# Kernel optimization log

Hardware: AMD Instinct MI355X
Metric: run time of the kernel (lower is better)

## Reference

```python
import jax, jax.numpy as jnp
import numpy as np

PATCH = 4
WINDOW = 4
MAX_ROUNDS = 4
MIN_ROUNDS = 2
LAMBDA_P = 0.2
TOPK = 8


def _ln(x, g, b, eps=1e-5):
    m = x.mean(-1, keepdims=True)
    v = ((x - m) ** 2).mean(-1, keepdims=True)
    return (x - m) / jnp.sqrt(v + eps) * g + b


def _mlp(x, w1, b1, w2, b2):
    # Linear -> exact GELU -> Linear (matches nn.GELU default)
    return jax.nn.gelu(x @ w1 + b1, approximate=False) @ w2 + b2


def setup_inputs() -> dict:
    key = jax.random.key(0)
    ks = jax.random.split(key, 24)
    B, T, D, V = 16, 4096, 256, 256
    s = 0.02
    w = lambda i, shape: jax.random.normal(ks[i], shape, jnp.float32) * s
    z = lambda *shape: jnp.zeros(shape, jnp.float32)
    o = lambda *shape: jnp.ones(shape, jnp.float32)
    return {
        'x': jax.random.randint(ks[0], (B, T), 0, V),
        'emb': w(1, (V, D)), 'pos': w(2, (PATCH, D)),
        'gru_wih': w(3, (D, 3 * D)), 'gru_whh': w(4, (D, 3 * D)),
        'gru_bih': z(3 * D), 'gru_bhh': z(3 * D),
        'ln_p_g': o(D), 'ln_p_b': z(D),
        'sum_w': w(5, (D, D)), 'sum_b': z(D),
        'msg_w1': w(6, (2 * D, D)), 'msg_b1': z(D), 'msg_w2': w(7, (D, D)), 'msg_b2': z(D),
        'upd_w1': w(8, (2 * D, D)), 'upd_b1': z(D), 'upd_w2': w(9, (D, D)), 'upd_b2': z(D),
        'halt_w': w(10, (D, 1)), 'halt_b': z(1),
        'ln_mp_g': o(D), 'ln_mp_b': z(D),
        'q_w': w(11, (D, D)), 'q_b': z(D),
        'k_w': w(12, (D, D)), 'k_b': z(D),
        'v_w': w(13, (D, D)), 'v_b': z(D),
        'o_w': w(14, (D, D)), 'o_b': z(D),
        'bc_w': w(15, (D, D)), 'bc_b': z(D),
        'ln_f_g': o(D), 'ln_f_b': z(D),
        'head_w': w(16, (D, V)),
    }


def reference(x, emb, pos, gru_wih, gru_whh, gru_bih, gru_bhh, ln_p_g, ln_p_b,
              sum_w, sum_b, msg_w1, msg_b1, msg_w2, msg_b2, upd_w1, upd_b1,
              upd_w2, upd_b2, halt_w, halt_b, ln_mp_g, ln_mp_b, q_w, q_b,
              k_w, k_b, v_w, v_b, o_w, o_b, bc_w, bc_b, ln_f_g, ln_f_b, head_w):
    B, T = x.shape
    D = emb.shape[1]
    Np = T // PATCH  # T is divisible by PATCH for these shapes (no pad needed)

    # --- GRU patch processor over B*Np sequences of length PATCH ---
    tok = x.reshape(B * Np, PATCH)
    hseq = emb[tok] + pos[None]  # [BN, P, D]

    def gru_step(h, xt):
        gi = xt @ gru_wih + gru_bih
        gh = h @ gru_whh + gru_bhh
        ir, iz, inn = jnp.split(gi, 3, -1)
        hr, hz, hn = jnp.split(gh, 3, -1)
        r = jax.nn.sigmoid(ir + hr)
        zz = jax.nn.sigmoid(iz + hz)
        n = jnp.tanh(inn + r * hn)
        h = (1 - zz) * n + zz * h
        return h, h

    h0 = jnp.zeros((B * Np, D), hseq.dtype)
    _, gout = jax.lax.scan(gru_step, h0, jnp.swapaxes(hseq, 0, 1))
    local = _ln(jnp.swapaxes(gout, 0, 1), ln_p_g, ln_p_b).reshape(B, Np, PATCH, D)
    summaries = local.mean(2) @ sum_w + sum_b  # [B, Np, D]

    # --- Local message passing with ACT-style halting (fixed MAX_ROUNDS) ---
    h = summaries
    remaining = jnp.ones((B, Np, 1), h.dtype)
    out_mp = jnp.zeros_like(h)
    kl = jnp.zeros((), h.dtype)
    for step in range(MAX_ROUNDS):
        padded = jnp.pad(h, ((0, 0), (WINDOW, 0), (0, 0)))
        # neighbors: self plus previous WINDOW patches -> [B, Np, W+1, D]
        neigh = jnp.stack([padded[:, WINDOW - w:WINDOW - w + Np] for w in range(WINDOW + 1)], axis=2)
        self_exp = jnp.broadcast_to(h[:, :, None, :], neigh.shape)
        msgs = _mlp(jnp.concatenate([self_exp, neigh], -1), msg_w1, msg_b1, msg_w2, msg_b2).mean(2)
        h = _ln(h + _mlp(jnp.concatenate([h, msgs], -1), upd_w1, upd_b1, upd_w2, upd_b2), ln_mp_g, ln_mp_b)
        if step < MIN_ROUNDS:
            hp = jnp.zeros((B, Np, 1), h.dtype)
        else:
            hp = jax.nn.sigmoid(h.mean(1, keepdims=True) @ halt_w + halt_b)  # [B,1,1]
            hp = jnp.broadcast_to(hp, (B, Np, 1))
        if step == MAX_ROUNDS - 1:
            hp = jnp.ones_like(hp)
        out_mp = out_mp + remaining * hp * h
        remaining = remaining * (1 - hp)
        p_geom = LAMBDA_P * (1 - LAMBDA_P) ** step
        # F.kl_div(log(mean+eps), log(p_geom), log_target=True) = p*(log p - log(mean+eps))
        kl = kl + p_geom * (np.log(p_geom) - jnp.log(hp.mean() + 1e-8))
    kl = kl / MAX_ROUNDS

    # --- Sparse top-k causal retrieval ---
    q = out_mp @ q_w + q_b
    kk = out_mp @ k_w + k_b
    v = out_mp @ v_w + v_b
    scores = jnp.einsum('bnd,bmd->bnm', q, kk) / np.sqrt(D).astype(np.float32)
    causal = jnp.tril(jnp.ones((Np, Np), bool))
    neg = jnp.asarray(-jnp.inf, scores.dtype)
    scores = jnp.where(causal[None], scores, neg)
    vals, idx = jax.lax.top_k(scores, TOPK)  # [B, Np, k]
    bi = jnp.arange(B)[:, None, None]
    ni = jnp.arange(Np)[None, :, None]
    sparse = jnp.full_like(scores, neg).at[bi, ni, idx].set(vals)
    attn = jax.nn.softmax(sparse, axis=-1)
    retrieved = jnp.einsum('bnm,bmd->bnd', attn, v) @ o_w + o_b

    # --- Broadcast back to tokens and project ---
    combined = out_mp + retrieved
    broad = combined @ bc_w + bc_b
    final = (local + broad[:, :, None, :]).reshape(B, Np * PATCH, D)[:, :T]
    logits = _ln(final, ln_f_g, ln_f_b) @ head_w
    return logits, kl
```

## Files before the change

### kernel.cpp

```cpp
#include <hip/hip_runtime.h>
#include <math.h>


typedef __bf16 bf16_t;
typedef bf16_t bf16x8 __attribute__((ext_vector_type(8)));
typedef bf16_t bf16x4 __attribute__((ext_vector_type(4)));
typedef float f32x4 __attribute__((ext_vector_type(4)));

#define GF_BIAS 1
#define GF_GELU 4
#define GF_RES 8
#define GF_F32OUT 32

__device__ __forceinline__ float gelu_exact(float x) {
  return 0.5f * x * (1.0f + erff(x * 0.7071067811865475f));
}

__device__ __forceinline__ float sigm(float x) { return 1.f / (1.f + expf(-x)); }

__device__ __forceinline__ float wave_sum(float v) {
#pragma unroll
  for (int o = 32; o; o >>= 1) v += __shfl_xor(v, o, 64);
  return v;
}

__device__ __forceinline__ void gload16(const void* g, void* l) {
  __builtin_amdgcn_global_load_lds(
      (const __attribute__((address_space(1))) void*)g,
      (__attribute__((address_space(3))) void*)l, 16, 0, 0);
}

__device__ __forceinline__ unsigned long long skey(float s, int m) {
  unsigned u = __float_as_uint(s);
  u ^= (u & 0x80000000u) ? 0xFFFFFFFFu : 0x80000000u;
  return ((unsigned long long)u << 32) | (unsigned)(0x7FFFFFFF - m);
}

template<int FLAGS>
__global__ __launch_bounds__(256)
void gemm_bt(const bf16_t* __restrict__ A, const bf16_t* __restrict__ Bt,
             void* __restrict__ Cv, const float* __restrict__ bias,
             const bf16_t* __restrict__ res,
             int lda, int ldb, int ldc, int ldr)
{
  __shared__ __align__(16) bf16_t As[128][64];
  __shared__ __align__(16) bf16_t Bs[128][64];
  const int m0 = blockIdx.x * 128, n0 = blockIdx.y * 128;
  const int tid = threadIdx.x, lane = tid & 63, wave = tid >> 6;
  const int wm = (wave >> 1) << 6, wn = (wave & 1) << 6;
  const int lr = lane & 15, lg = lane >> 4;
  const int cx = lane & 7;

  const int srow = wave * 32 + (lane >> 3);
  const int scol = (((lane & 7) ^ ((lane >> 3) & 7)) * 8);
  const bf16_t* ga = A  + (long long)(m0 + srow) * lda + scol;
  const bf16_t* gb = Bt + (long long)(n0 + srow) * ldb + scol;
  char* lA = (char*)(&As[srow][0]) + (lane & 7) * 16;
  char* lB = (char*)(&Bs[srow][0]) + (lane & 7) * 16;

  f32x4 acc[4][4] = {};

#pragma unroll
  for (int kt = 0; kt < 4; kt++) {
    const int ko = kt * 64;
#pragma unroll
    for (int q = 0; q < 4; q++) {
      gload16(ga + (long long)q * 8 * lda + ko, lA + q * 1024);
      gload16(gb + (long long)q * 8 * ldb + ko, lB + q * 1024);
    }
    __syncthreads();
#pragma unroll
    for (int kk = 0; kk < 2; kk++) {
      const int co = ((kk * 4 + lg) ^ cx) << 4;
      bf16x8 af[4], bfv[4];
#pragma unroll
      for (int i = 0; i < 4; i++)
        af[i]  = *(const bf16x8*)((char*)As + (wm + i * 16 + lr) * 128 + co);
#pragma unroll
      for (int j = 0; j < 4; j++)
        bfv[j] = *(const bf16x8*)((char*)Bs + (wn + j * 16 + lr) * 128 + co);
#pragma unroll
      for (int i = 0; i < 4; i++)
#pragma unroll
        for (int j = 0; j < 4; j++)
          acc[i][j] = __builtin_amdgcn_mfma_f32_16x16x32_bf16(af[i], bfv[j], acc[i][j], 0, 0, 0);
    }
    if (kt < 3) __syncthreads();
  }

#pragma unroll
  for (int i = 0; i < 4; i++) {
#pragma unroll
    for (int j = 0; j < 4; j++) {
      const int col = n0 + wn + j * 16 + lr;
      const float bval = (FLAGS & GF_BIAS) ? bias[col] : 0.f;
#pragma unroll
      for (int e = 0; e < 4; e++) {
        const int row = m0 + wm + i * 16 + lg * 4 + e;
        float v = acc[i][j][e] + bval;
        if (FLAGS & GF_RES) v += (float)res[(long long)row * ldr + col];
        if (FLAGS & GF_GELU) v = gelu_exact(v);
        const long long ci = (long long)row * ldc + col;
        if (FLAGS & GF_F32OUT) ((float*)Cv)[ci] = v;
        else                   ((bf16_t*)Cv)[ci] = (bf16_t)v;
      }
    }
  }
}

template<int FLAGS>
__global__ __launch_bounds__(256)
void gemm64(const bf16_t* __restrict__ A, const bf16_t* __restrict__ Bt,
            void* __restrict__ Cv, const float* __restrict__ bias,
            const bf16_t* __restrict__ res,
            int lda, int ldb, int ldc, int ldr)
{
  __shared__ __align__(16) bf16_t As[64][64];
  __shared__ __align__(16) bf16_t Bs[64][64];
  const int m0 = blockIdx.x * 64, n0 = blockIdx.y * 64;
  const int tid = threadIdx.x, lane = tid & 63, wave = tid >> 6;
  const int wm = (wave >> 1) * 32, wn = (wave & 1) * 32;
  const int lr = lane & 15, lg = lane >> 4;
  const int cx = lane & 7;

  const int srow = tid >> 3;
  const int scol = (((tid & 7) ^ (srow & 7)) * 8);
  const bf16_t* ga = A  + (long long)(m0 + srow) * lda + scol;
  const bf16_t* gb = Bt + (long long)(n0 + srow) * ldb + scol;
  char* lA = (char*)As + tid * 16;
  char* lB = (char*)Bs + tid * 16;

  f32x4 acc[2][2] = {};

#pragma unroll
  for (int kt = 0; kt < 4; kt++) {
    const int ko = kt * 64;
    gload16(ga + ko, lA);
    gload16(ga + 32LL * lda + ko, lA + 4096);
    gload16(gb + ko, lB);
    gload16(gb + 32LL * ldb + ko, lB + 4096);
    __syncthreads();
#pragma unroll
    for (int kk = 0; kk < 2; kk++) {
      const int co = ((kk * 4 + lg) ^ cx) << 4;
      bf16x8 af[2], bfv[2];
#pragma unroll
      for (int i = 0; i < 2; i++)
        af[i]  = *(const bf16x8*)((char*)As + (wm + i * 16 + lr) * 128 + co);
#pragma unroll
      for (int j = 0; j < 2; j++)
        bfv[j] = *(const bf16x8*)((char*)Bs + (wn + j * 16 + lr) * 128 + co);
#pragma unroll
      for (int i = 0; i < 2; i++)
#pragma unroll
        for (int j = 0; j < 2; j++)
          acc[i][j] = __builtin_amdgcn_mfma_f32_16x16x32_bf16(af[i], bfv[j], acc[i][j], 0, 0, 0);
    }
    if (kt < 3) __syncthreads();
  }

#pragma unroll
  for (int i = 0; i < 2; i++) {
#pragma unroll
    for (int j = 0; j < 2; j++) {
      const int col = n0 + wn + j * 16 + lr;
      const float bval = (FLAGS & GF_BIAS) ? bias[col] : 0.f;
#pragma unroll
      for (int e = 0; e < 4; e++) {
        const int row = m0 + wm + i * 16 + lg * 4 + e;
        float v = acc[i][j][e] + bval;
        if (FLAGS & GF_RES) v += (float)res[(long long)row * ldr + col];
        if (FLAGS & GF_GELU) v = gelu_exact(v);
        const long long ci = (long long)row * ldc + col;
        if (FLAGS & GF_F32OUT) ((float*)Cv)[ci] = v;
        else                   ((bf16_t*)Cv)[ci] = (bf16_t)v;
      }
    }
  }
}

__global__ __launch_bounds__(256)
void k_fatopk(const bf16_t* __restrict__ QKV, bf16_t* __restrict__ O) {
  __shared__ unsigned long long cand[4][16][8];
  __shared__ float wrow[16][8];
  __shared__ int   irow[16][8];
  const int b = blockIdx.y;
  const int qw = (int)((blockIdx.x + ((unsigned)(b * 21) & 63u)) & 63u);
  const int tid = threadIdx.x;
  const int wid = tid >> 6;
  const int lane = tid & 63;
  const int lr = lane & 15, lg = lane >> 4;
  const bf16_t* Qp = QKV + (long long)b * (1024LL * 768);
  const bf16_t* Kp = Qp + 256;
  const bf16_t* Vp = Qp + 512;
  const int q0 = qw * 16;
  const int qrow = q0 + lr;

  bf16x8 bq[8];
#pragma unroll
  for (int s = 0; s < 8; s++)
    bq[s] = *(const bf16x8*)(Qp + (long long)qrow * 768 + s * 32 + lg * 8);

  unsigned long long kv[8] = {0ull, 0ull, 0ull, 0ull, 0ull, 0ull, 0ull, 0ull};

#define INS8(KEY) {                                                     \
    const unsigned long long k_ = (KEY);                                \
    if (k_ > kv[7]) {                                                   \
      kv[7] = k_;                                                       \
      _Pragma("unroll")                                                 \
      for (int j_ = 7; j_ > 0; j_--)                                    \
        if (kv[j_] > kv[j_-1]) {                                        \
          const unsigned long long t_ = kv[j_];                         \
          kv[j_] = kv[j_-1]; kv[j_-1] = t_;                             \
        }                                                               \
    }                                                                   \
  }

  const int klim = qw + 1;
  for (int kt = wid; kt < klim; kt += 4) {
    const bf16_t* ka = Kp + (long long)(kt * 16 + lr) * 768 + lg * 8;
    bf16x8 af[8];
#pragma unroll
    for (int s = 0; s < 8; s++) af[s] = *(const bf16x8*)(ka + s * 32);
    f32x4 a0 = {}, a1 = {};
#pragma unroll
    for (int s = 0; s < 8; s += 2) {
      a0 = __builtin_amdgcn_mfma_f32_16x16x32_bf16(af[s],     bq[s],     a0, 0, 0, 0);
      a1 = __builtin_amdgcn_mfma_f32_16x16x32_bf16(af[s + 1], bq[s + 1], a1, 0, 0, 0);
    }
#pragma unroll
    for (int e = 0; e < 4; e++) {
      const int m = kt * 16 + lg * 4 + e;
      if (m <= qrow) INS8(skey((a0[e] + a1[e]) * 0.0625f, m));
    }
  }
#undef INS8

#pragma unroll
  for (int r = 0; r < 8; r++) {
    unsigned long long mk = kv[0];
    unsigned long long ok = __shfl_xor(mk, 16, 64); if (ok > mk) mk = ok;
    ok = __shfl_xor(mk, 32, 64); if (ok > mk) mk = ok;
    if (lg == 0) cand[wid][lr][r] = mk;
    if (kv[0] == mk && mk != 0ull) {
#pragma unroll
      for (int j = 0; j < 7; j++) kv[j] = kv[j + 1];
      kv[7] = 0ull;
    }
  }
  __syncthreads();

  if (wid == 0) {
    unsigned long long kv2[8];
#pragma unroll
    for (int j = 0; j < 8; j++) kv2[j] = cand[lg][lr][j];
    float wv[8]; int wi[8];
#pragma unroll
    for (int r = 0; r < 8; r++) {
      unsigned long long mk = kv2[0];
      unsigned long long ok = __shfl_xor(mk, 16, 64); if (ok > mk) mk = ok;
      ok = __shfl_xor(mk, 32, 64); if (ok > mk) mk = ok;
      if (mk != 0ull) {
        unsigned hi = (unsigned)(mk >> 32);
        hi ^= (hi & 0x80000000u) ? 0x80000000u : 0xFFFFFFFFu;
        wv[r] = __uint_as_float(hi);
        wi[r] = 0x7FFFFFFF - (int)(unsigned)(mk & 0xFFFFFFFFu);
      } else {
        wv[r] = 0.f; wi[r] = -1;
      }
      if (kv2[0] == mk && mk != 0ull) {
#pragma unroll
        for (int j = 0; j < 7; j++) kv2[j] = kv2[j + 1];
        kv2[7] = 0ull;
      }
    }
    const float mx = wv[0];
    float w8[8]; float den = 0.f;
#pragma unroll
    for (int j = 0; j < 8; j++) {
      w8[j] = (wi[j] >= 0) ? expf(wv[j] - mx) : 0.f;
      den += w8[j];
    }
    const float inv = 1.f / den;
    if (lg == 0) {
#pragma unroll
      for (int j = 0; j < 8; j++) {
        wrow[lr][j] = w8[j] * inv;
        irow[lr][j] = wi[j];
      }
    }
  }
  __syncthreads();

  const int rr = wid * 4 + lg;
  const int c0 = (lane & 15) * 16;
  f32x4 av[4] = {};
#pragma unroll
  for (int j = 0; j < 8; j++) {
    const int idx = irow[rr][j];
    if (idx >= 0) {
      const float wj = wrow[rr][j];
      const bf16_t* vr = Vp + (long long)idx * 768 + c0;
      const bf16x8 v0 = *(const bf16x8*)vr;
      const bf16x8 v1 = *(const bf16x8*)(vr + 8);
#pragma unroll
      for (int e = 0; e < 4; e++) {
        av[0][e] = fmaf(wj, (float)v0[e],     av[0][e]);
        av[1][e] = fmaf(wj, (float)v0[4 + e], av[1][e]);
        av[2][e] = fmaf(wj, (float)v1[e],     av[2][e]);
        av[3][e] = fmaf(wj, (float)v1[4 + e], av[3][e]);
      }
    }
  }
  bf16_t* op = O + ((long long)b * 1024 + q0 + rr) * 256 + c0;
  bf16x8 o0, o1;
#pragma unroll
  for (int e = 0; e < 4; e++) {
    o0[e] = (bf16_t)av[0][e]; o0[4 + e] = (bf16_t)av[1][e];
    o1[e] = (bf16_t)av[2][e]; o1[4 + e] = (bf16_t)av[3][e];
  }
  *(bf16x8*)op = o0;
  *(bf16x8*)(op + 8) = o1;
}

struct TD { const float* src; bf16_t* dst; int N; int k0; int ld; };
struct PrepArgs {
  TD d[16];
  const float* emb; const float* pos; bf16_t* XE;
  const float* msg_b1; const float* msg_b2; const float* upd_w1; const float* upd_b1;
  const float* q_b; const float* k_b; const float* v_b;
  float* BIAS3; float* QKVB;
};

__global__ __launch_bounds__(256) void k_prep(PrepArgs pa) {
  const int y = blockIdx.y, x = blockIdx.x, d = threadIdx.x;
  if (y < 16) {
    TD t = pa.d[y];
    if (x >= t.N) return;
    if (t.k0 < 0) t.dst[(long long)x * 256 + d] = (bf16_t)t.src[(long long)x * t.ld + d];
    else          t.dst[(long long)x * 256 + d] = (bf16_t)t.src[(long long)(t.k0 + d) * t.ld + x];
  } else if (y == 16) {
    const int p = x >> 8, v = x & 255;
    pa.XE[(long long)x * 256 + d] = (bf16_t)(pa.emb[v * 256 + d] + pa.pos[p * 256 + d]);
  } else {
    if      (x == 0) pa.BIAS3[d] = pa.msg_b1[d];
    else if (x == 1) pa.BIAS3[256 + d] = 0.f;
    else if (x == 2) {
      float acc = pa.upd_b1[d];
      for (int k = 0; k < 256; k++) acc += pa.msg_b2[k] * pa.upd_w1[(long long)(256 + k) * 256 + d];
      pa.BIAS3[512 + d] = acc;
    }
    else if (x == 3) pa.QKVB[d] = pa.q_b[d];
    else if (x == 4) pa.QKVB[256 + d] = pa.k_b[d];
    else if (x == 5) pa.QKVB[512 + d] = pa.v_b[d];
  }
}

__global__ __launch_bounds__(64)
void k_gru_gate(const int* __restrict__ x, const bf16_t* __restrict__ gitab,
                const bf16_t* __restrict__ GH, const float* __restrict__ bhh,
                bf16_t* __restrict__ H, bf16_t* __restrict__ LOC, int t)
{
  const int s = blockIdx.x, lane = threadIdx.x, d0 = lane * 4;
  const int v = x[s * 4 + t];
  const bf16_t* gi = gitab + (long long)(t * 256 + v) * 768;
  const bf16x4 g_r = *(const bf16x4*)(gi + d0);
  const bf16x4 g_z = *(const bf16x4*)(gi + 256 + d0);
  const bf16x4 g_n = *(const bf16x4*)(gi + 512 + d0);
  float hr[4], hz[4], hn[4], hp[4];
  if (t == 0) {
#pragma unroll
    for (int e = 0; e < 4; e++) {
      hr[e] = bhh[d0 + e]; hz[e] = bhh[256 + d0 + e]; hn[e] = bhh[512 + d0 + e];
      hp[e] = 0.f;
    }
  } else {
    const bf16_t* gh = GH + (long long)s * 768;
    const bf16x4 a = *(const bf16x4*)(gh + d0);
    const bf16x4 b4 = *(const bf16x4*)(gh + 256 + d0);
    const bf16x4 c4 = *(const bf16x4*)(gh + 512 + d0);
    const bf16x4 hv = *(const bf16x4*)(H + (long long)s * 256 + d0);
#pragma unroll
    for (int e = 0; e < 4; e++) { hr[e] = a[e]; hz[e] = b4[e]; hn[e] = c4[e]; hp[e] = hv[e]; }
  }
  bf16x4 ho;
#pragma unroll
  for (int e = 0; e < 4; e++) {
    const float r = sigm((float)g_r[e] + hr[e]);
    const float zz = sigm((float)g_z[e] + hz[e]);
    const float nn = tanhf((float)g_n[e] + r * hn[e]);
    ho[e] = (bf16_t)((1.f - zz) * nn + zz * hp[e]);
  }
  *(bf16x4*)(H + (long long)s * 256 + d0) = ho;
  *(bf16x4*)(LOC + ((long long)s * 4 + t) * 256 + d0) = ho;
}

__global__ __launch_bounds__(64)
void k_ln(const bf16_t* __restrict__ X, const bf16_t* __restrict__ ADD, int addmode,
          bf16_t* __restrict__ OUT, const float* __restrict__ g,
          const float* __restrict__ b)
{
  const long long r = blockIdx.x;
  const int d0 = threadIdx.x * 4;
  const bf16x4 xv = *(const bf16x4*)(X + r * 256 + d0);
  float xf[4];
#pragma unroll
  for (int e = 0; e < 4; e++) xf[e] = (float)xv[e];
  if (addmode == 1) {
    const bf16x4 av = *(const bf16x4*)(ADD + r * 256 + d0);
#pragma unroll
    for (int e = 0; e < 4; e++) xf[e] += (float)av[e];
  } else if (addmode == 2) {
    const bf16x4 av = *(const bf16x4*)(ADD + (r >> 2) * 256 + d0);
#pragma unroll
    for (int e = 0; e < 4; e++) xf[e] += (float)av[e];
  }
  const float mean = wave_sum(xf[0] + xf[1] + xf[2] + xf[3]) * (1.f / 256.f);
  float q = 0.f;
#pragma unroll
  for (int e = 0; e < 4; e++) { const float dx = xf[e] - mean; q += dx * dx; }
  const float rstd = rsqrtf(wave_sum(q) * (1.f / 256.f) + 1e-5f);
  const float4 gv = *(const float4*)(g + d0);
  const float4 bv = *(const float4*)(b + d0);
  const float gg[4] = {gv.x, gv.y, gv.z, gv.w};
  const float bb[4] = {bv.x, bv.y, bv.z, bv.w};
  bf16x4 ov;
#pragma unroll
  for (int e = 0; e < 4; e++) ov[e] = (bf16_t)((xf[e] - mean) * rstd * gg[e] + bb[e]);
  *(bf16x4*)(OUT + r * 256 + d0) = ov;
}

__global__ __launch_bounds__(64)
void k_ln_out(const bf16_t* __restrict__ X, const bf16_t* __restrict__ ADD,
              bf16_t* __restrict__ OUTMP, const float* __restrict__ HP,
              const float* __restrict__ g, const float* __restrict__ b)
{
  const long long r = blockIdx.x;
  const int d0 = threadIdx.x * 4;
  const bf16x4 xv = *(const bf16x4*)(X + r * 256 + d0);
  const bf16x4 avv = *(const bf16x4*)(ADD + r * 256 + d0);
  float xf[4];
#pragma unroll
  for (int e = 0; e < 4; e++) xf[e] = (float)xv[e] + (float)avv[e];
  const float mean = wave_sum(xf[0] + xf[1] + xf[2] + xf[3]) * (1.f / 256.f);
  float q = 0.f;
#pragma unroll
  for (int e = 0; e < 4; e++) { const float dx = xf[e] - mean; q += dx * dx; }
  const float rstd = rsqrtf(wave_sum(q) * (1.f / 256.f) + 1e-5f);
  const float4 gv = *(const float4*)(g + d0);
  const float4 bv = *(const float4*)(b + d0);
  const float gg[4] = {gv.x, gv.y, gv.z, gv.w};
  const float bb[4] = {bv.x, bv.y, bv.z, bv.w};
  const float rem = 1.f - HP[(int)(r >> 10)];
  const bf16x4 pv = *(const bf16x4*)(OUTMP + r * 256 + d0);
  bf16x4 ov;
#pragma unroll
  for (int e = 0; e < 4; e++) {
    const float y = (xf[e] - mean) * rstd * gg[e] + bb[e];
    ov[e] = (bf16_t)((float)pv[e] + rem * y);
  }
  *(bf16x4*)(OUTMP + r * 256 + d0) = ov;
}

__global__ __launch_bounds__(64)
void k_lnp4(bf16_t* __restrict__ LOC, bf16_t* __restrict__ SUMB,
            const float* __restrict__ g, const float* __restrict__ b)
{
  const long long s = blockIdx.x;
  const int d0 = threadIdx.x * 4;
  const float4 gv = *(const float4*)(g + d0);
  const float4 bv = *(const float4*)(b + d0);
  const float gg[4] = {gv.x, gv.y, gv.z, gv.w};
  const float bb[4] = {bv.x, bv.y, bv.z, bv.w};
  float accd[4] = {0.f, 0.f, 0.f, 0.f};
#pragma unroll
  for (int t = 0; t < 4; t++) {
    bf16_t* row = LOC + (s * 4 + t) * 256 + d0;
    const bf16x4 xv = *(const bf16x4*)row;
    float xf[4];
#pragma unroll
    for (int e = 0; e < 4; e++) xf[e] = (float)xv[e];
    const float mean = wave_sum(xf[0] + xf[1] + xf[2] + xf[3]) * (1.f / 256.f);
    float q = 0.f;
#pragma unroll
    for (int e = 0; e < 4; e++) { const float dx = xf[e] - mean; q += dx * dx; }
    const float rstd = rsqrtf(wave_sum(q) * (1.f / 256.f) + 1e-5f);
    bf16x4 ov;
#pragma unroll
    for (int e = 0; e < 4; e++) {
      const float y = (xf[e] - mean) * rstd * gg[e] + bb[e];
      ov[e] = (bf16_t)y;
      accd[e] += y;
    }
    *(bf16x4*)row = ov;
  }
  bf16x4 sv;
#pragma unroll
  for (int e = 0; e < 4; e++) sv[e] = (bf16_t)(accd[e] * 0.25f);
  *(bf16x4*)(SUMB + s * 256 + d0) = sv;
}

__global__ __launch_bounds__(64)
void k_gelumix(const bf16_t* __restrict__ A3, bf16_t* __restrict__ G)
{
  const long long s = blockIdx.x;
  const int n = (int)(s & 1023);
  const int d0 = threadIdx.x * 4;
  const bf16x4 av = *(const bf16x4*)(A3 + s * 768 + d0);
  float a[4];
#pragma unroll
  for (int e = 0; e < 4; e++) a[e] = (float)av[e];
  float acc[4] = {0.f, 0.f, 0.f, 0.f};
  const bf16_t* bbase = A3 + s * 768 + 256 + d0;
#pragma unroll
  for (int w = 0; w <= 4; w++) {
    if (n >= w) {
      const bf16x4 bn = *(const bf16x4*)(bbase - (long long)w * 768);
#pragma unroll
      for (int e = 0; e < 4; e++) acc[e] += gelu_exact(a[e] + (float)bn[e]);
    } else {
#pragma unroll
      for (int e = 0; e < 4; e++) acc[e] += gelu_exact(a[e]);
    }
  }
  bf16x4 ov;
#pragma unroll
  for (int e = 0; e < 4; e++) ov[e] = (bf16_t)(acc[e] * 0.2f);
  *(bf16x4*)(G + s * 256 + d0) = ov;
}

__global__ __launch_bounds__(64)
void k_halt1(const bf16_t* __restrict__ Hm, float* __restrict__ PS) {
  const int c = blockIdx.x, b = blockIdx.y, d0 = threadIdx.x * 4;
  float acc[4] = {0.f, 0.f, 0.f, 0.f};
  const bf16_t* base = Hm + ((long long)b * 1024 + c * 32) * 256 + d0;
#pragma unroll 4
  for (int n = 0; n < 32; n++) {
    const bf16x4 hv = *(const bf16x4*)(base + (long long)n * 256);
#pragma unroll
    for (int e = 0; e < 4; e++) acc[e] += (float)hv[e];
  }
  float4 o4; o4.x = acc[0]; o4.y = acc[1]; o4.z = acc[2]; o4.w = acc[3];
  *(float4*)(PS + ((long long)b * 32 + c) * 256 + d0) = o4;
}

__global__ __launch_bounds__(64)
void k_halt2(const float* __restrict__ PS, const float* __restrict__ hw,
             const float* __restrict__ hb, float* __restrict__ HP) {
  const int b = blockIdx.x, d0 = threadIdx.x * 4;
  float acc[4] = {0.f, 0.f, 0.f, 0.f};
  for (int c = 0; c < 32; c++) {
    const float4 p4 = *(const float4*)(PS + ((long long)b * 32 + c) * 256 + d0);
    acc[0] += p4.x; acc[1] += p4.y; acc[2] += p4.z; acc[3] += p4.w;
  }
  const float4 w4 = *(const float4*)(hw + d0);
  float val = (acc[0] * w4.x + acc[1] * w4.y + acc[2] * w4.z + acc[3] * w4.w) * (1.f / 1024.f);
  val = wave_sum(val);
  if (threadIdx.x == 0) HP[b] = sigm(val + hb[0]);
}

__global__ void k_kl(const float* __restrict__ HP, float* __restrict__ out) {
  float s = 0.f;
  for (int b = 0; b < 16; b++) s += HP[b];
  const float hpm = s * (1.f / 16.f);
  const float l8 = logf(1e-8f);
  const float p0 = 0.2f, p1 = 0.16f, p2 = 0.128f, p3 = 0.1024f;
  const float kl = p0 * (logf(p0) - l8)
                 + p1 * (logf(p1) - l8)
                 + p2 * (logf(p2) - logf(hpm + 1e-8f))
                 + p3 * (logf(p3) - logf(1.f + 1e-8f));
  out[0] = kl * 0.25f;
}

__global__ __launch_bounds__(64)
void k_outmp(const bf16_t* __restrict__ Hm, const float* __restrict__ HP,
             bf16_t* __restrict__ O, int acc) {
  const long long s = blockIdx.x;
  const int d0 = threadIdx.x * 4;
  const int b = (int)(s >> 10);
  const float hp = HP[b];
  const bf16x4 hv = *(const bf16x4*)(Hm + s * 256 + d0);
  bf16x4 ov;
  if (acc) {
    const bf16x4 pv = *(const bf16x4*)(O + s * 256 + d0);
#pragma unroll
    for (int e = 0; e < 4; e++) ov[e] = (bf16_t)((float)pv[e] + (1.f - hp) * (float)hv[e]);
  } else {
#pragma unroll
    for (int e = 0; e < 4; e++) ov[e] = (bf16_t)(hp * (float)hv[e]);
  }
  *(bf16x4*)(O + s * 256 + d0) = ov;
}

extern "C" void kernel_launch(void* const* d_in, const int* in_sizes, int n_in,
                              void* d_out, int out_size, void* d_ws, size_t ws_size,
                              hipStream_t stream) {
  (void)in_sizes; (void)n_in; (void)ws_size;
  const int*   x      = (const int*)d_in[0];
  const float* emb    = (const float*)d_in[1];
  const float* pos    = (const float*)d_in[2];
  const float* wih    = (const float*)d_in[3];
  const float* whh    = (const float*)d_in[4];
  const float* bih    = (const float*)d_in[5];
  const float* bhh    = (const float*)d_in[6];
  const float* lnp_g  = (const float*)d_in[7];
  const float* lnp_b  = (const float*)d_in[8];
  const float* sum_w  = (const float*)d_in[9];
  const float* sum_b  = (const float*)d_in[10];
  const float* msg_w1 = (const float*)d_in[11];
  const float* msg_b1 = (const float*)d_in[12];
  const float* msg_w2 = (const float*)d_in[13];
  const float* msg_b2 = (const float*)d_in[14];
  const float* upd_w1 = (const float*)d_in[15];
  const float* upd_b1 = (const float*)d_in[16];
  const float* upd_w2 = (const float*)d_in[17];
  const float* upd_b2 = (const float*)d_in[18];
  const float* halt_w = (const float*)d_in[19];
  const float* halt_b = (const float*)d_in[20];
  const float* lnm_g  = (const float*)d_in[21];
  const float* lnm_b  = (const float*)d_in[22];
  const float* q_b    = (const float*)d_in[24];
  const float* k_b    = (const float*)d_in[26];
  const float* v_b    = (const float*)d_in[28];
  const float* o_b    = (const float*)d_in[30];
  const float* bc_b   = (const float*)d_in[32];
  const float* lnf_g  = (const float*)d_in[33];
  const float* lnf_b  = (const float*)d_in[34];

  char* base = (char*)d_ws;
  size_t off = 0;
  auto alloc = [&](size_t bytes) -> void* {
    void* p = (void*)(base + off);
    off += (bytes + 255) & ~(size_t)255;
    return p;
  };
  const size_t SL2 = 16384ull * 256 * 2;
  bf16_t* WIHT  = (bf16_t*)alloc(768 * 256 * 2);
  bf16_t* WHHT  = (bf16_t*)alloc(768 * 256 * 2);
  bf16_t* SUMT  = (bf16_t*)alloc(256 * 256 * 2);
  bf16_t* MW    = (bf16_t*)alloc(768 * 256 * 2);
  bf16_t* W2T   = (bf16_t*)alloc(256 * 256 * 2);
  bf16_t* W2NT  = (bf16_t*)alloc(256 * 256 * 2);
  bf16_t* UW1MT = (bf16_t*)alloc(256 * 256 * 2);
  bf16_t* UW2T  = (bf16_t*)alloc(256 * 256 * 2);
  bf16_t* WCB   = (bf16_t*)alloc(256 * 256 * 2);
  bf16_t* QKVW  = (bf16_t*)alloc(768 * 256 * 2);
  bf16_t* OT    = (bf16_t*)alloc(256 * 256 * 2);
  bf16_t* BCT   = (bf16_t*)alloc(256 * 256 * 2);
  bf16_t* HEADT = (bf16_t*)alloc(256 * 256 * 2);
  float*  BIAS3 = (float*)alloc(768 * 4);
  float*  QKVB  = (float*)alloc(768 * 4);
  bf16_t* XE    = (bf16_t*)alloc(1024ull * 256 * 2);
  bf16_t* GITAB = (bf16_t*)alloc(1024ull * 768 * 2);
  bf16_t* LOCb  = (bf16_t*)alloc(65536ull * 256 * 2);

  char*   SCR   = (char*)alloc(16ull * 1024 * 1024 * 4);
  bf16_t* GH    = (bf16_t*)SCR;
  bf16_t* H     = (bf16_t*)(SCR + 25165824);
  bf16_t* SUMB  = (bf16_t*)(SCR + 33554432);
  bf16_t* A3    = (bf16_t*)(SCR + 41943040);

  bf16_t* HMP   = (bf16_t*)alloc(SL2);
  bf16_t* G     = (bf16_t*)alloc(SL2);
  bf16_t* BROAD = (bf16_t*)alloc(SL2);
  bf16_t* UB    = (bf16_t*)alloc(SL2);
  bf16_t* U2B   = (bf16_t*)alloc(SL2);
  bf16_t* OUTMP = (bf16_t*)alloc(SL2);
  bf16_t* QKV   = (bf16_t*)alloc(16384ull * 768 * 2);
  float*  PS    = (float*)alloc(512ull * 256 * 4);
  float*  HP    = (float*)alloc(64);
  bf16_t* ATT   = UB;
  bf16_t* COMB  = U2B;
  float*  out   = (float*)d_out;
  float*  klout = out + (out_size - 1);

  PrepArgs pa;
  pa.d[0]  = { wih,                    WIHT,            768, 0,   768 };
  pa.d[1]  = { whh,                    WHHT,            768, 0,   768 };
  pa.d[2]  = { sum_w,                  SUMT,            256, 0,   256 };
  pa.d[3]  = { msg_w1,                 MW,              256, 0,   256 };
  pa.d[4]  = { msg_w1,                 MW + 256 * 256,  256, 256, 256 };
  pa.d[5]  = { upd_w1,                 MW + 512 * 256,  256, 0,   256 };
  pa.d[6]  = { msg_w2,                 W2T,             256, 0,   256 };
  pa.d[7]  = { upd_w1,                 UW1MT,           256, 256, 256 };
  pa.d[8]  = { upd_w2,                 UW2T,            256, 0,   256 };
  pa.d[9]  = { (const float*)d_in[23], QKVW,            256, 0,   256 };
  pa.d[10] = { (const float*)d_in[25], QKVW + 256*256,  256, 0,   256 };
  pa.d[11] = { (const float*)d_in[27], QKVW + 512*256,  256, 0,   256 };
  pa.d[12] = { (const float*)d_in[29], OT,              256, 0,   256 };
  pa.d[13] = { (const float*)d_in[31], BCT,             256, 0,   256 };
  pa.d[14] = { (const float*)d_in[35], HEADT,           256, 0,   256 };
  pa.d[15] = { msg_w2,                 W2NT,            256, -1,  256 };
  pa.emb = emb; pa.pos = pos; pa.XE = XE;
  pa.msg_b1 = msg_b1; pa.msg_b2 = msg_b2; pa.upd_w1 = upd_w1; pa.upd_b1 = upd_b1;
  pa.q_b = q_b; pa.k_b = k_b; pa.v_b = v_b;
  pa.BIAS3 = BIAS3; pa.QKVB = QKVB;
  k_prep<<<dim3(1024, 18), 256, 0, stream>>>(pa);

  gemm64<0><<<dim3(4, 4), 256, 0, stream>>>(
      UW1MT, W2NT, WCB, nullptr, nullptr, 256, 256, 256, 0);

  gemm64<GF_BIAS><<<dim3(16, 12), 256, 0, stream>>>(
      XE, WIHT, GITAB, bih, nullptr, 256, 256, 768, 0);

  k_gru_gate<<<16384, 64, 0, stream>>>(x, GITAB, GH, bhh, H, LOCb, 0);
  for (int t = 1; t < 4; t++) {
    gemm_bt<GF_BIAS><<<dim3(128, 6), 256, 0, stream>>>(
        H, WHHT, GH, bhh, nullptr, 256, 256, 768, 0);
    k_gru_gate<<<16384, 64, 0, stream>>>(x, GITAB, GH, bhh, H, LOCb, t);
  }

  k_lnp4<<<16384, 64, 0, stream>>>(LOCb, SUMB, lnp_g, lnp_b);
  gemm64<GF_BIAS><<<dim3(256, 4), 256, 0, stream>>>(
      SUMB, SUMT, HMP, sum_b, nullptr, 256, 256, 256, 0);

  for (int step = 0; step < 4; step++) {
    gemm_bt<GF_BIAS><<<dim3(128, 6), 256, 0, stream>>>(
        HMP, MW, A3, BIAS3, nullptr, 256, 256, 768, 0);
    k_gelumix<<<16384, 64, 0, stream>>>(A3, G);
    gemm64<GF_RES | GF_GELU><<<dim3(256, 4), 256, 0, stream>>>(
        G, WCB, UB, nullptr, A3 + 512, 256, 256, 256, 768);
    gemm64<GF_BIAS><<<dim3(256, 4), 256, 0, stream>>>(
        UB, UW2T, U2B, upd_b2, nullptr, 256, 256, 256, 0);
    if (step == 3) {
      k_ln_out<<<16384, 64, 0, stream>>>(HMP, U2B, OUTMP, HP, lnm_g, lnm_b);
    } else {
      k_ln<<<16384, 64, 0, stream>>>(HMP, U2B, 1, HMP, lnm_g, lnm_b);
      if (step == 2) {
        k_halt1<<<dim3(32, 16), 64, 0, stream>>>(HMP, PS);
        k_halt2<<<16, 64, 0, stream>>>(PS, halt_w, halt_b, HP);
        k_kl<<<1, 1, 0, stream>>>(HP, klout);
        k_outmp<<<16384, 64, 0, stream>>>(HMP, HP, OUTMP, 0);
      }
    }
  }

  gemm_bt<GF_BIAS><<<dim3(128, 6), 256, 0, stream>>>(
      OUTMP, QKVW, QKV, QKVB, nullptr, 256, 256, 768, 0);
  k_fatopk<<<dim3(64, 16), 256, 0, stream>>>(QKV, ATT);
  gemm64<GF_BIAS | GF_RES><<<dim3(256, 4), 256, 0, stream>>>(
      ATT, OT, COMB, o_b, OUTMP, 256, 256, 256, 256);
  gemm64<GF_BIAS><<<dim3(256, 4), 256, 0, stream>>>(
      COMB, BCT, BROAD, bc_b, nullptr, 256, 256, 256, 0);

  k_ln<<<65536, 64, 0, stream>>>(LOCb, BROAD, 2, LOCb, lnf_g, lnf_b);
  gemm_bt<GF_F32OUT><<<dim3(512, 2), 256, 0, stream>>>(
      LOCb, HEADT, out, nullptr, nullptr, 256, 256, 256, 0);
}
```

Measured before the change: 467.9 us.

## Fuse update GEMM with LayerNorm, pair causal top-k tiles, merge halt/KL kernels

```diff
diff --git a/kernel.cpp b/kernel.cpp
--- a/kernel.cpp
+++ b/kernel.cpp
@@ -179,13 +179,142 @@
   }
 }
 
+template<int MODE>
+__global__ __launch_bounds__(256)
+void gemm_ln(const bf16_t* __restrict__ A, const bf16_t* __restrict__ Bt,
+             bf16_t* __restrict__ C, const float* __restrict__ bias,
+             const float* __restrict__ g, const float* __restrict__ bvec,
+             bf16_t* __restrict__ OUTMP, const float* __restrict__ HP)
+{
+  __shared__ __align__(16) bf16_t As[64][64];
+  __shared__ __align__(16) bf16_t Bs[256][64];
+  __shared__ float redsum[4][64];
+  __shared__ float redsq[4][64];
+  const int m0 = blockIdx.x * 64;
+  const int tid = threadIdx.x, lane = tid & 63, w = tid >> 6;
+  const int lr = lane & 15, lg = lane >> 4, cx = lane & 7;
+
+  f32x4 acc[4][4] = {};
+
+#pragma unroll
+  for (int kt = 0; kt < 4; kt++) {
+    const int ko = kt * 64;
+    {
+      int cid = tid, r = cid >> 3, c = cid & 7;
+      gload16(A + (long long)(m0 + r) * 256 + ko + ((c ^ (r & 7)) * 8), (char*)As + cid * 16);
+      cid = tid + 256; r = cid >> 3; c = cid & 7;
+      gload16(A + (long long)(m0 + r) * 256 + ko + ((c ^ (r & 7)) * 8), (char*)As + cid * 16);
+    }
+#pragma unroll
+    for (int it = 0; it < 8; it++) {
+      const int cid = it * 256 + tid, r = cid >> 3, c = cid & 7;
+      gload16(Bt + (long long)r * 256 + ko + ((c ^ (r & 7)) * 8), (char*)Bs + cid * 16);
+    }
+    __syncthreads();
+#pragma unroll
+    for (int kk = 0; kk < 2; kk++) {
+      const int co = ((kk * 4 + lg) ^ cx) << 4;
+      bf16x8 af[4], bfv[4];
+#pragma unroll
+      for (int i = 0; i < 4; i++)
+        af[i]  = *(const bf16x8*)((char*)As + (i * 16 + lr) * 128 + co);
+#pragma unroll
+      for (int j = 0; j < 4; j++)
+        bfv[j] = *(const bf16x8*)((char*)Bs + (w * 64 + j * 16 + lr) * 128 + co);
+#pragma unroll
+      for (int i = 0; i < 4; i++)
+#pragma unroll
+        for (int j = 0; j < 4; j++)
+          acc[i][j] = __builtin_amdgcn_mfma_f32_16x16x32_bf16(af[i], bfv[j], acc[i][j], 0, 0, 0);
+    }
+    if (kt < 3) __syncthreads();
+  }
+
+  float v[4][4][4];
+  float rs[4][4], rq[4][4];
+#pragma unroll
+  for (int i = 0; i < 4; i++) {
+#pragma unroll
+    for (int e = 0; e < 4; e++) { rs[i][e] = 0.f; rq[i][e] = 0.f; }
+  }
+#pragma unroll
+  for (int i = 0; i < 4; i++) {
+#pragma unroll
+    for (int j = 0; j < 4; j++) {
+      const int col = w * 64 + j * 16 + lr;
+      const float bval = bias[col];
+#pragma unroll
+      for (int e = 0; e < 4; e++) {
+        const long long rg = m0 + i * 16 + lg * 4 + e;
+        const float val = acc[i][j][e] + bval + (float)C[rg * 256 + col];
+        v[i][j][e] = val;
+        rs[i][e] += val;
+        rq[i][e] += val * val;
+      }
+    }
+  }
+#pragma unroll
+  for (int off = 1; off < 16; off <<= 1) {
+#pragma unroll
+    for (int i = 0; i < 4; i++)
+#pragma unroll
+      for (int e = 0; e < 4; e++) {
+        rs[i][e] += __shfl_xor(rs[i][e], off, 64);
+        rq[i][e] += __shfl_xor(rq[i][e], off, 64);
+      }
+  }
+  if (lr == 0) {
+#pragma unroll
+    for (int i = 0; i < 4; i++)
+#pragma unroll
+      for (int e = 0; e < 4; e++) {
+        redsum[w][i * 16 + lg * 4 + e] = rs[i][e];
+        redsq[w][i * 16 + lg * 4 + e]  = rq[i][e];
+      }
+  }
+  __syncthreads();
+  float mean[4][4], rstd[4][4];
+#pragma unroll
+  for (int i = 0; i < 4; i++) {
+#pragma unroll
+    for (int e = 0; e < 4; e++) {
+      const int r = i * 16 + lg * 4 + e;
+      const float S = redsum[0][r] + redsum[1][r] + redsum[2][r] + redsum[3][r];
+      const float Q = redsq[0][r] + redsq[1][r] + redsq[2][r] + redsq[3][r];
+      const float m = S * (1.f / 256.f);
+      float var = Q * (1.f / 256.f) - m * m;
+      if (var < 0.f) var = 0.f;
+      mean[i][e] = m;
+      rstd[i][e] = rsqrtf(var + 1e-5f);
+    }
+  }
+#pragma unroll
+  for (int i = 0; i < 4; i++) {
+#pragma unroll
+    for (int j = 0; j < 4; j++) {
+      const int col = w * 64 + j * 16 + lr;
+      const float gg = g[col], bb = bvec[col];
+#pragma unroll
+      for (int e = 0; e < 4; e++) {
+        const long long rg = m0 + i * 16 + lg * 4 + e;
+        const float y = (v[i][j][e] - mean[i][e]) * rstd[i][e] * gg + bb;
+        if (MODE == 0) {
+          C[rg * 256 + col] = (bf16_t)y;
+        } else {
+          const float rem = 1.f - HP[(int)(rg >> 10)];
+          OUTMP[rg * 256 + col] = (bf16_t)((float)OUTMP[rg * 256 + col] + rem * y);
+        }
+      }
+    }
+  }
+}
+
 __global__ __launch_bounds__(256)
 void k_fatopk(const bf16_t* __restrict__ QKV, bf16_t* __restrict__ O) {
   __shared__ unsigned long long cand[4][16][8];
   __shared__ float wrow[16][8];
   __shared__ int   irow[16][8];
   const int b = blockIdx.y;
-  const int qw = (int)((blockIdx.x + ((unsigned)(b * 21) & 63u)) & 63u);
   const int tid = threadIdx.x;
   const int wid = tid >> 6;
   const int lane = tid & 63;
@@ -193,15 +322,18 @@
   const bf16_t* Qp = QKV + (long long)b * (1024LL * 768);
   const bf16_t* Kp = Qp + 256;
   const bf16_t* Vp = Qp + 512;
-  const int q0 = qw * 16;
-  const int qrow = q0 + lr;
-
-  bf16x8 bq[8];
-#pragma unroll
-  for (int s = 0; s < 8; s++)
-    bq[s] = *(const bf16x8*)(Qp + (long long)qrow * 768 + s * 32 + lg * 8);
-
-  unsigned long long kv[8] = {0ull, 0ull, 0ull, 0ull, 0ull, 0ull, 0ull, 0ull};
+
+  for (int half = 0; half < 2; half++) {
+    const int qw = (half == 0) ? (int)blockIdx.x : 63 - (int)blockIdx.x;
+    const int q0 = qw * 16;
+    const int qrow = q0 + lr;
+
+    bf16x8 bq[8];
+#pragma unroll
+    for (int s = 0; s < 8; s++)
+      bq[s] = *(const bf16x8*)(Qp + (long long)qrow * 768 + s * 32 + lg * 8);
+
+    unsigned long long kv[8] = {0ull, 0ull, 0ull, 0ull, 0ull, 0ull, 0ull, 0ull};
 
 #define INS8(KEY) {                                                     \
     const unsigned long long k_ = (KEY);                                \
@@ -216,111 +348,113 @@
     }                                                                   \
   }
 
-  const int klim = qw + 1;
-  for (int kt = wid; kt < klim; kt += 4) {
-    const bf16_t* ka = Kp + (long long)(kt * 16 + lr) * 768 + lg * 8;
-    bf16x8 af[8];
-#pragma unroll
-    for (int s = 0; s < 8; s++) af[s] = *(const bf16x8*)(ka + s * 32);
-    f32x4 a0 = {}, a1 = {};
-#pragma unroll
-    for (int s = 0; s < 8; s += 2) {
-      a0 = __builtin_amdgcn_mfma_f32_16x16x32_bf16(af[s],     bq[s],     a0, 0, 0, 0);
-      a1 = __builtin_amdgcn_mfma_f32_16x16x32_bf16(af[s + 1], bq[s + 1], a1, 0, 0, 0);
-    }
-#pragma unroll
-    for (int e = 0; e < 4; e++) {
-      const int m = kt * 16 + lg * 4 + e;
-      if (m <= qrow) INS8(skey((a0[e] + a1[e]) * 0.0625f, m));
-    }
-  }
+    const int klim = qw + 1;
+    for (int kt = wid; kt < klim; kt += 4) {
+      const bf16_t* ka = Kp + (long long)(kt * 16 + lr) * 768 + lg * 8;
+      bf16x8 af[8];
+#pragma unroll
+      for (int s = 0; s < 8; s++) af[s] = *(const bf16x8*)(ka + s * 32);
+      f32x4 a0 = {}, a1 = {};
+#pragma unroll
+      for (int s = 0; s < 8; s += 2) {
+        a0 = __builtin_amdgcn_mfma_f32_16x16x32_bf16(af[s],     bq[s],     a0, 0, 0, 0);
+        a1 = __builtin_amdgcn_mfma_f32_16x16x32_bf16(af[s + 1], bq[s + 1], a1, 0, 0, 0);
+      }
+#pragma unroll
+      for (int e = 0; e < 4; e++) {
+        const int m = kt * 16 + lg * 4 + e;
+        if (m <= qrow) INS8(skey((a0[e] + a1[e]) * 0.0625f, m));
+      }
+    }
 #undef INS8
 
 #pragma unroll
-  for (int r = 0; r < 8; r++) {
-    unsigned long long mk = kv[0];
-    unsigned long long ok = __shfl_xor(mk, 16, 64); if (ok > mk) mk = ok;
-    ok = __shfl_xor(mk, 32, 64); if (ok > mk) mk = ok;
-    if (lg == 0) cand[wid][lr][r] = mk;
-    if (kv[0] == mk && mk != 0ull) {
-#pragma unroll
-      for (int j = 0; j < 7; j++) kv[j] = kv[j + 1];
-      kv[7] = 0ull;
-    }
-  }
-  __syncthreads();
-
-  if (wid == 0) {
-    unsigned long long kv2[8];
-#pragma unroll
-    for (int j = 0; j < 8; j++) kv2[j] = cand[lg][lr][j];
-    float wv[8]; int wi[8];
-#pragma unroll
     for (int r = 0; r < 8; r++) {
-      unsigned long long mk = kv2[0];
+      unsigned long long mk = kv[0];
       unsigned long long ok = __shfl_xor(mk, 16, 64); if (ok > mk) mk = ok;
       ok = __shfl_xor(mk, 32, 64); if (ok > mk) mk = ok;
-      if (mk != 0ull) {
-        unsigned hi = (unsigned)(mk >> 32);
-        hi ^= (hi & 0x80000000u) ? 0x80000000u : 0xFFFFFFFFu;
-        wv[r] = __uint_as_float(hi);
-        wi[r] = 0x7FFFFFFF - (int)(unsigned)(mk & 0xFFFFFFFFu);
-      } else {
-        wv[r] = 0.f; wi[r] = -1;
-      }
-      if (kv2[0] == mk && mk != 0ull) {
-#pragma unroll
-        for (int j = 0; j < 7; j++) kv2[j] = kv2[j + 1];
-        kv2[7] = 0ull;
-      }
-    }
-    const float mx = wv[0];
-    float w8[8]; float den = 0.f;
+      if (lg == 0) cand[wid][lr][r] = mk;
+      if (kv[0] == mk && mk != 0ull) {
+#pragma unroll
+        for (int j = 0; j < 7; j++) kv[j] = kv[j + 1];
+        kv[7] = 0ull;
+      }
+    }
+    __syncthreads();
+
+    if (wid == 0) {
+      unsigned long long kv2[8];
+#pragma unroll
+      for (int j = 0; j < 8; j++) kv2[j] = cand[lg][lr][j];
+      float wv[8]; int wi[8];
+#pragma unroll
+      for (int r = 0; r < 8; r++) {
+        unsigned long long mk = kv2[0];
+        unsigned long long ok = __shfl_xor(mk, 16, 64); if (ok > mk) mk = ok;
+        ok = __shfl_xor(mk, 32, 64); if (ok > mk) mk = ok;
+        if (mk != 0ull) {
+          unsigned hi = (unsigned)(mk >> 32);
+          hi ^= (hi & 0x80000000u) ? 0x80000000u : 0xFFFFFFFFu;
+          wv[r] = __uint_as_float(hi);
+          wi[r] = 0x7FFFFFFF - (int)(unsigned)(mk & 0xFFFFFFFFu);
+        } else {
+          wv[r] = 0.f; wi[r] = -1;
+        }
+        if (kv2[0] == mk && mk != 0ull) {
+#pragma unroll
+          for (int j = 0; j < 7; j++) kv2[j] = kv2[j + 1];
+          kv2[7] = 0ull;
+        }
+      }
+      const float mx = wv[0];
+      float w8[8]; float den = 0.f;
+#pragma unroll
+      for (int j = 0; j < 8; j++) {
+        w8[j] = (wi[j] >= 0) ? expf(wv[j] - mx) : 0.f;
+        den += w8[j];
+      }
+      const float inv = 1.f / den;
+      if (lg == 0) {
+#pragma unroll
+        for (int j = 0; j < 8; j++) {
+          wrow[lr][j] = w8[j] * inv;
+          irow[lr][j] = wi[j];
+        }
+      }
+    }
+    __syncthreads();
+
+    const int rr = wid * 4 + lg;
+    const int c0 = (lane & 15) * 16;
+    f32x4 av[4] = {};
 #pragma unroll
     for (int j = 0; j < 8; j++) {
-      w8[j] = (wi[j] >= 0) ? expf(wv[j] - mx) : 0.f;
-      den += w8[j];
-    }
-    const float inv = 1.f / den;
-    if (lg == 0) {
-#pragma unroll
-      for (int j = 0; j < 8; j++) {
-        wrow[lr][j] = w8[j] * inv;
-        irow[lr][j] = wi[j];
-      }
-    }
-  }
-  __syncthreads();
-
-  const int rr = wid * 4 + lg;
-  const int c0 = (lane & 15) * 16;
-  f32x4 av[4] = {};
-#pragma unroll
-  for (int j = 0; j < 8; j++) {
-    const int idx = irow[rr][j];
-    if (idx >= 0) {
-      const float wj = wrow[rr][j];
-      const bf16_t* vr = Vp + (long long)idx * 768 + c0;
-      const bf16x8 v0 = *(const bf16x8*)vr;
-      const bf16x8 v1 = *(const bf16x8*)(vr + 8);
-#pragma unroll
-      for (int e = 0; e < 4; e++) {
-        av[0][e] = fmaf(wj, (float)v0[e],     av[0][e]);
-        av[1][e] = fmaf(wj, (float)v0[4 + e], av[1][e]);
-        av[2][e] = fmaf(wj, (float)v1[e],     av[2][e]);
-        av[3][e] = fmaf(wj, (float)v1[4 + e], av[3][e]);
-      }
-    }
-  }
-  bf16_t* op = O + ((long long)b * 1024 + q0 + rr) * 256 + c0;
-  bf16x8 o0, o1;
-#pragma unroll
-  for (int e = 0; e < 4; e++) {
-    o0[e] = (bf16_t)av[0][e]; o0[4 + e] = (bf16_t)av[1][e];
-    o1[e] = (bf16_t)av[2][e]; o1[4 + e] = (bf16_t)av[3][e];
-  }
-  *(bf16x8*)op = o0;
-  *(bf16x8*)(op + 8) = o1;
+      const int idx = irow[rr][j];
+      if (idx >= 0) {
+        const float wj = wrow[rr][j];
+        const bf16_t* vr = Vp + (long long)idx * 768 + c0;
+        const bf16x8 v0 = *(const bf16x8*)vr;
+        const bf16x8 v1 = *(const bf16x8*)(vr + 8);
+#pragma unroll
+        for (int e = 0; e < 4; e++) {
+          av[0][e] = fmaf(wj, (float)v0[e],     av[0][e]);
+          av[1][e] = fmaf(wj, (float)v0[4 + e], av[1][e]);
+          av[2][e] = fmaf(wj, (float)v1[e],     av[2][e]);
+          av[3][e] = fmaf(wj, (float)v1[4 + e], av[3][e]);
+        }
+      }
+    }
+    bf16_t* op = O + ((long long)b * 1024 + q0 + rr) * 256 + c0;
+    bf16x8 o0, o1;
+#pragma unroll
+    for (int e = 0; e < 4; e++) {
+      o0[e] = (bf16_t)av[0][e]; o0[4 + e] = (bf16_t)av[1][e];
+      o1[e] = (bf16_t)av[2][e]; o1[4 + e] = (bf16_t)av[3][e];
+    }
+    *(bf16x8*)op = o0;
+    *(bf16x8*)(op + 8) = o1;
+    if (half == 0) __syncthreads();
+  }
 }
 
 struct TD { const float* src; bf16_t* dst; int N; int k0; int ld; };
@@ -431,38 +565,6 @@
 }
 
 __global__ __launch_bounds__(64)
-void k_ln_out(const bf16_t* __restrict__ X, const bf16_t* __restrict__ ADD,
-              bf16_t* __restrict__ OUTMP, const float* __restrict__ HP,
-              const float* __restrict__ g, const float* __restrict__ b)
-{
-  const long long r = blockIdx.x;
-  const int d0 = threadIdx.x * 4;
-  const bf16x4 xv = *(const bf16x4*)(X + r * 256 + d0);
-  const bf16x4 avv = *(const bf16x4*)(ADD + r * 256 + d0);
-  float xf[4];
-#pragma unroll
-  for (int e = 0; e < 4; e++) xf[e] = (float)xv[e] + (float)avv[e];
-  const float mean = wave_sum(xf[0] + xf[1] + xf[2] + xf[3]) * (1.f / 256.f);
-  float q = 0.f;
-#pragma unroll
-  for (int e = 0; e < 4; e++) { const float dx = xf[e] - mean; q += dx * dx; }
-  const float rstd = rsqrtf(wave_sum(q) * (1.f / 256.f) + 1e-5f);
-  const float4 gv = *(const float4*)(g + d0);
-  const float4 bv = *(const float4*)(b + d0);
-  const float gg[4] = {gv.x, gv.y, gv.z, gv.w};
-  const float bb[4] = {bv.x, bv.y, bv.z, bv.w};
-  const float rem = 1.f - HP[(int)(r >> 10)];
-  const bf16x4 pv = *(const bf16x4*)(OUTMP + r * 256 + d0);
-  bf16x4 ov;
-#pragma unroll
-  for (int e = 0; e < 4; e++) {
-    const float y = (xf[e] - mean) * rstd * gg[e] + bb[e];
-    ov[e] = (bf16_t)((float)pv[e] + rem * y);
-  }
-  *(bf16x4*)(OUTMP + r * 256 + d0) = ov;
-}
-
-__global__ __launch_bounds__(64)
 void k_lnp4(bf16_t* __restrict__ LOC, bf16_t* __restrict__ SUMB,
             const float* __restrict__ g, const float* __restrict__ b)
 {
@@ -544,10 +646,12 @@
   *(float4*)(PS + ((long long)b * 32 + c) * 256 + d0) = o4;
 }
 
-__global__ __launch_bounds__(64)
-void k_halt2(const float* __restrict__ PS, const float* __restrict__ hw,
-             const float* __restrict__ hb, float* __restrict__ HP) {
-  const int b = blockIdx.x, d0 = threadIdx.x * 4;
+__global__ __launch_bounds__(1024)
+void k_halt2kl(const float* __restrict__ PS, const float* __restrict__ hw,
+               const float* __restrict__ hb, float* __restrict__ HP,
+               float* __restrict__ out) {
+  __shared__ float sh[16];
+  const int b = threadIdx.x >> 6, lane = threadIdx.x & 63, d0 = lane * 4;
   float acc[4] = {0.f, 0.f, 0.f, 0.f};
   for (int c = 0; c < 32; c++) {
     const float4 p4 = *(const float4*)(PS + ((long long)b * 32 + c) * 256 + d0);
@@ -556,20 +660,24 @@
   const float4 w4 = *(const float4*)(hw + d0);
   float val = (acc[0] * w4.x + acc[1] * w4.y + acc[2] * w4.z + acc[3] * w4.w) * (1.f / 1024.f);
   val = wave_sum(val);
-  if (threadIdx.x == 0) HP[b] = sigm(val + hb[0]);
-}
-
-__global__ void k_kl(const float* __restrict__ HP, float* __restrict__ out) {
-  float s = 0.f;
-  for (int b = 0; b < 16; b++) s += HP[b];
-  const float hpm = s * (1.f / 16.f);
-  const float l8 = logf(1e-8f);
-  const float p0 = 0.2f, p1 = 0.16f, p2 = 0.128f, p3 = 0.1024f;
-  const float kl = p0 * (logf(p0) - l8)
-                 + p1 * (logf(p1) - l8)
-                 + p2 * (logf(p2) - logf(hpm + 1e-8f))
-                 + p3 * (logf(p3) - logf(1.f + 1e-8f));
-  out[0] = kl * 0.25f;
+  if (lane == 0) {
+    const float hp = sigm(val + hb[0]);
+    HP[b] = hp;
+    sh[b] = hp;
+  }
+  __syncthreads();
+  if (threadIdx.x == 0) {
+    float s = 0.f;
+    for (int bb = 0; bb < 16; bb++) s += sh[bb];
+    const float hpm = s * (1.f / 16.f);
+    const float l8 = logf(1e-8f);
+    const float p0 = 0.2f, p1 = 0.16f, p2 = 0.128f, p3 = 0.1024f;
+    const float kl = p0 * (logf(p0) - l8)
+                   + p1 * (logf(p1) - l8)
+                   + p2 * (logf(p2) - logf(hpm + 1e-8f))
+                   + p3 * (logf(p3) - logf(1.f + 1e-8f));
+    out[0] = kl * 0.25f;
+  }
 }
 
 __global__ __launch_bounds__(64)
@@ -720,16 +828,15 @@
     k_gelumix<<<16384, 64, 0, stream>>>(A3, G);
     gemm64<GF_RES | GF_GELU><<<dim3(256, 4), 256, 0, stream>>>(
         G, WCB, UB, nullptr, A3 + 512, 256, 256, 256, 768);
-    gemm64<GF_BIAS><<<dim3(256, 4), 256, 0, stream>>>(
-        UB, UW2T, U2B, upd_b2, nullptr, 256, 256, 256, 0);
     if (step == 3) {
-      k_ln_out<<<16384, 64, 0, stream>>>(HMP, U2B, OUTMP, HP, lnm_g, lnm_b);
+      gemm_ln<1><<<256, 256, 0, stream>>>(
+          UB, UW2T, HMP, upd_b2, lnm_g, lnm_b, OUTMP, HP);
     } else {
-      k_ln<<<16384, 64, 0, stream>>>(HMP, U2B, 1, HMP, lnm_g, lnm_b);
+      gemm_ln<0><<<256, 256, 0, stream>>>(
+          UB, UW2T, HMP, upd_b2, lnm_g, lnm_b, nullptr, nullptr);
       if (step == 2) {
         k_halt1<<<dim3(32, 16), 64, 0, stream>>>(HMP, PS);
-        k_halt2<<<16, 64, 0, stream>>>(PS, halt_w, halt_b, HP);
-        k_kl<<<1, 1, 0, stream>>>(HP, klout);
+        k_halt2kl<<<1, 1024, 0, stream>>>(PS, halt_w, halt_b, HP, klout);
         k_outmp<<<16384, 64, 0, stream>>>(HMP, HP, OUTMP, 0);
       }
     }
@@ -737,7 +844,7 @@
 
   gemm_bt<GF_BIAS><<<dim3(128, 6), 256, 0, stream>>>(
       OUTMP, QKVW, QKV, QKVB, nullptr, 256, 256, 768, 0);
-  k_fatopk<<<dim3(64, 16), 256, 0, stream>>>(QKV, ATT);
+  k_fatopk<<<dim3(32, 16), 256, 0, stream>>>(QKV, ATT);
   gemm64<GF_BIAS | GF_RES><<<dim3(256, 4), 256, 0, stream>>>(
       ATT, OT, COMB, o_b, OUTMP, 256, 256, 256, 256);
   gemm64<GF_BIAS><<<dim3(256, 4), 256, 0, stream>>>(
```

After: 470.2 us. About the same (+0.5%).
